# Kernel tuning notes

Hardware: AMD Instinct MI355X
Metric: run time of the kernel (lower is better)

Reference implementation:

```python
import jax, jax.numpy as jnp
import numpy as np

K_CONST = 2.0
KERNEL = 5
ALPHA = 1e-4
BETA = 0.75


def setup_inputs() -> dict:
    key = jax.random.key(0)
    x = jax.random.normal(key, (16, 96, 224, 224), dtype=jnp.float32)
    return {"x": x}


def reference(x) -> jnp.ndarray:
    # Original: y = conv2d(x^2, ones(C,C,5,5), pad=2); out = x / (k + alpha*y)**beta.
    # The all-ones C x C filter sums x^2 over ALL channels and a 5x5 window,
    # producing an identical map for every output channel. Compute that sum
    # once on a single-channel tensor and broadcast -- same math, O(C) cheaper.
    s = jnp.sum(x * x, axis=1, keepdims=True)  # [B,1,H,W] channel-summed squares
    w = jnp.ones((1, 1, KERNEL, KERNEL), dtype=x.dtype)
    y = jax.lax.conv_general_dilated(
        s, w, window_strides=(1, 1), padding="SAME",
        dimension_numbers=("NCHW", "OIHW", "NCHW"),
    )  # [B,1,H,W], broadcasts against [B,C,H,W]
    return x / (K_CONST + ALPHA * y) ** BETA
```

## Files before the change

### kernel.cpp

```cpp
#include <hip/hip_runtime.h>
#include <math.h>


#define BB 16
#define CC 96
#define HH 224
#define WW 224
#define HW (HH * WW)
#define CHW (CC * HW)
#define NPIX (BB * HW)
#define W4 (WW / 4)
#define NCOL (BB * HH * W4)

__global__ __launch_bounds__(256) void lrn_sqsum(const float* __restrict__ x,
                                                 float* __restrict__ s) {
    int t = blockIdx.x * blockDim.x + threadIdx.x;
    if (t >= NCOL) return;
    int w4 = t % W4;
    int bh = t / W4;
    int b  = bh / HH;
    int h  = bh % HH;
    size_t idx = (((size_t)b * CHW + (size_t)h * WW) >> 2) + w4;
    const float4* xp = (const float4*)x;
    float4 acc = make_float4(0.f, 0.f, 0.f, 0.f);
#pragma unroll 4
    for (int c = 0; c < CC; ++c) {
        float4 v = xp[idx + (size_t)c * (HW / 4)];
        acc.x += v.x * v.x;
        acc.y += v.y * v.y;
        acc.z += v.z * v.z;
        acc.w += v.w * v.w;
    }
    ((float4*)s)[t] = acc;
}

__global__ __launch_bounds__(256) void lrn_scale(const float* __restrict__ s,
                                                 float* __restrict__ sc) {
    int t = blockIdx.x * blockDim.x + threadIdx.x;
    if (t >= NPIX) return;
    int w  = t % WW;
    int bh = t / WW;
    int h  = bh % HH;
    float y = 0.f;
#pragma unroll
    for (int dh = -2; dh <= 2; ++dh) {
        int hh = h + dh;
        if (hh < 0 || hh >= HH) continue;
        const float* row = s + (size_t)(bh + dh) * WW;
#pragma unroll
        for (int dw = -2; dw <= 2; ++dw) {
            int ww = w + dw;
            if (ww >= 0 && ww < WW) y += row[ww];
        }
    }
    sc[t] = powf(2.0f + 1e-4f * y, -0.75f);
}

__global__ __launch_bounds__(256) void lrn_norm(const float* __restrict__ x,
                                                const float* __restrict__ sc,
                                                float* __restrict__ out) {
    int t = blockIdx.x * blockDim.x + threadIdx.x;
    if (t >= NCOL) return;
    int w4 = t % W4;
    int bh = t / W4;
    int b  = bh / HH;
    int h  = bh % HH;
    float4 scv = ((const float4*)sc)[t];
    size_t idx = (((size_t)b * CHW + (size_t)h * WW) >> 2) + w4;
    const float4* xp = (const float4*)x;
    float4* op = (float4*)out;
#pragma unroll 4
    for (int c = 0; c < CC; ++c) {
        size_t i = idx + (size_t)c * (HW / 4);
        float4 v = xp[i];
        v.x *= scv.x;
        v.y *= scv.y;
        v.z *= scv.z;
        v.w *= scv.w;
        op[i] = v;
    }
}

extern "C" void kernel_launch(void* const* d_in, const int* in_sizes, int n_in,
                              void* d_out, int out_size, void* d_ws, size_t ws_size,
                              hipStream_t stream) {
    const float* x = (const float*)d_in[0];
    float* out = (float*)d_out;
    float* s  = (float*)d_ws;
    float* sc = s + NPIX;

    lrn_sqsum<<<(NCOL + 255) / 256, 256, 0, stream>>>(x, s);
    lrn_scale<<<(NPIX + 255) / 256, 256, 0, stream>>>(s, sc);
    lrn_norm<<<(NCOL + 255) / 256, 256, 0, stream>>>(x, sc, out);
}
```

Before: 592.9 us.

## Split channel reduction and normalization across four channel groups with nontemporal accesses

The channel-sum and normalize kernels now launch a second grid dimension over four channel groups, so each thread handles a quarter of the channels and more threads are in flight. Partial sums go to a workspace buffer and are combined by a new small reduction kernel. Loads and stores of x and out use nontemporal builtins, and unrolling is raised. The cost is extra workspace traffic for the partials plus one more kernel launch.

```diff
diff --git a/kernel.cpp b/kernel.cpp
--- a/kernel.cpp
+++ b/kernel.cpp
@@ -11,32 +11,47 @@
 #define NPIX (BB * HW)
 #define W4 (WW / 4)
 #define NCOL (BB * HH * W4)
+#define CG 4
+#define CPG (CC / CG)
+
+typedef float v4f __attribute__((ext_vector_type(4)));
 
 __global__ __launch_bounds__(256) void lrn_sqsum(const float* __restrict__ x,
-                                                 float* __restrict__ s) {
-    int t = blockIdx.x * blockDim.x + threadIdx.x;
+                                                 float* __restrict__ part) {
+    int t  = blockIdx.x * 256 + threadIdx.x;
     if (t >= NCOL) return;
+    int cg = blockIdx.y;
     int w4 = t % W4;
     int bh = t / W4;
     int b  = bh / HH;
     int h  = bh % HH;
-    size_t idx = (((size_t)b * CHW + (size_t)h * WW) >> 2) + w4;
-    const float4* xp = (const float4*)x;
-    float4 acc = make_float4(0.f, 0.f, 0.f, 0.f);
-#pragma unroll 4
-    for (int c = 0; c < CC; ++c) {
-        float4 v = xp[idx + (size_t)c * (HW / 4)];
-        acc.x += v.x * v.x;
-        acc.y += v.y * v.y;
-        acc.z += v.z * v.z;
-        acc.w += v.w * v.w;
+    size_t idx = (((size_t)b * CHW + (size_t)h * WW) >> 2) + w4
+               + (size_t)cg * CPG * (HW / 4);
+    const v4f* xp = (const v4f*)x;
+    v4f acc = (v4f)(0.f);
+#pragma unroll 8
+    for (int c = 0; c < CPG; ++c) {
+        v4f v = __builtin_nontemporal_load(&xp[idx + (size_t)c * (HW / 4)]);
+        acc += v * v;
     }
-    ((float4*)s)[t] = acc;
+    ((v4f*)part)[(size_t)cg * NCOL + t] = acc;
+}
+
+__global__ __launch_bounds__(256) void lrn_sum4(const float* __restrict__ part,
+                                                float* __restrict__ s) {
+    int t = blockIdx.x * 256 + threadIdx.x;
+    if (t >= NCOL) return;
+    const v4f* p = (const v4f*)part;
+    v4f a = p[t];
+    v4f b = p[(size_t)NCOL + t];
+    v4f c = p[(size_t)2 * NCOL + t];
+    v4f d = p[(size_t)3 * NCOL + t];
+    ((v4f*)s)[t] = (a + b) + (c + d);
 }
 
 __global__ __launch_bounds__(256) void lrn_scale(const float* __restrict__ s,
                                                  float* __restrict__ sc) {
-    int t = blockIdx.x * blockDim.x + threadIdx.x;
+    int t = blockIdx.x * 256 + threadIdx.x;
     if (t >= NPIX) return;
     int w  = t % WW;
     int bh = t / WW;
@@ -59,25 +74,23 @@
 __global__ __launch_bounds__(256) void lrn_norm(const float* __restrict__ x,
                                                 const float* __restrict__ sc,
                                                 float* __restrict__ out) {
-    int t = blockIdx.x * blockDim.x + threadIdx.x;
+    int t  = blockIdx.x * 256 + threadIdx.x;
     if (t >= NCOL) return;
+    int cg = blockIdx.y;
     int w4 = t % W4;
     int bh = t / W4;
     int b  = bh / HH;
     int h  = bh % HH;
-    float4 scv = ((const float4*)sc)[t];
-    size_t idx = (((size_t)b * CHW + (size_t)h * WW) >> 2) + w4;
-    const float4* xp = (const float4*)x;
-    float4* op = (float4*)out;
-#pragma unroll 4
-    for (int c = 0; c < CC; ++c) {
+    v4f scv = ((const v4f*)sc)[t];
+    size_t idx = (((size_t)b * CHW + (size_t)h * WW) >> 2) + w4
+               + (size_t)cg * CPG * (HW / 4);
+    const v4f* xp = (const v4f*)x;
+    v4f* op = (v4f*)out;
+#pragma unroll 8
+    for (int c = 0; c < CPG; ++c) {
         size_t i = idx + (size_t)c * (HW / 4);
-        float4 v = xp[i];
-        v.x *= scv.x;
-        v.y *= scv.y;
-        v.z *= scv.z;
-        v.w *= scv.w;
-        op[i] = v;
+        v4f v = __builtin_nontemporal_load(&xp[i]);
+        __builtin_nontemporal_store(v * scv, &op[i]);
     }
 }
 
@@ -85,11 +98,13 @@
                               void* d_out, int out_size, void* d_ws, size_t ws_size,
                               hipStream_t stream) {
     const float* x = (const float*)d_in[0];
-    float* out = (float*)d_out;
-    float* s  = (float*)d_ws;
-    float* sc = s + NPIX;
+    float* out  = (float*)d_out;
+    float* part = (float*)d_ws;
+    float* s    = part + (size_t)CG * NPIX;
+    float* sc   = s + NPIX;
 
-    lrn_sqsum<<<(NCOL + 255) / 256, 256, 0, stream>>>(x, s);
+    lrn_sqsum<<<dim3((NCOL + 255) / 256, CG), 256, 0, stream>>>(x, part);
+    lrn_sum4 <<<(NCOL + 255) / 256, 256, 0, stream>>>(part, s);
     lrn_scale<<<(NPIX + 255) / 256, 256, 0, stream>>>(s, sc);
-    lrn_norm<<<(NCOL + 255) / 256, 256, 0, stream>>>(x, sc, out);
+    lrn_norm <<<dim3((NCOL + 255) / 256, CG), 256, 0, stream>>>(x, sc, out);
 }
```

Result: faster. 561.1 us (-5.4%).
